# Optimization experiments

Hardware: AMD Instinct MI355X
Metric: run time of the kernel (lower is better)

## Reference

```python
import jax, jax.numpy as jnp
import numpy as np

# MoE config (mirrors init_kwargs)
E = 8        # num_experts
K = 2        # num_experts_per_tok
H = 1024     # hidden_size
F = 2816     # moe_intermediate_size
B, S = 2, 512
NORM_TOPK = True


def setup_inputs() -> dict:
    key = jax.random.key(0)
    ks = jax.random.split(key, 5)
    x = jax.random.normal(ks[0], (B, S, H), dtype=jnp.float32)
    router_w = jax.random.normal(ks[1], (E, H), dtype=jnp.float32) * 0.02   # nn.Linear(H, E).weight
    gate_proj = jax.random.normal(ks[2], (E, H, F), dtype=jnp.float32) * 0.02
    up_proj = jax.random.normal(ks[3], (E, H, F), dtype=jnp.float32) * 0.02
    down_proj = jax.random.normal(ks[4], (E, F, H), dtype=jnp.float32) * 0.02
    return {"x": x, "router_w": router_w, "gate_proj": gate_proj,
            "up_proj": up_proj, "down_proj": down_proj}


def reference(x, router_w, gate_proj, up_proj, down_proj):
    b, s, h = x.shape
    xf = x.reshape(-1, h)                                    # [T, H]
    # Router: softmax over experts, top-k selection mask
    logits = xf @ router_w.T                                 # [T, E]
    probs = jax.nn.softmax(logits, axis=-1)
    topk_p, topk_i = jax.lax.top_k(probs, K)                 # [T, K]
    routing_map = jax.nn.one_hot(topk_i, E, dtype=probs.dtype).sum(axis=1)  # [T, E] 0/1
    if NORM_TOPK:
        probs = probs / topk_p.sum(-1, keepdims=True)
    weight = probs * routing_map                             # [T, E]; zero for unselected experts
    # Per-expert SwiGLU FFN; combine weighted by routing prob.
    # Dense-masked formulation: mathematically identical to the original
    # gather -> per-expert GEMM -> scatter_add, since weight==0 for unrouted pairs.
    g = jnp.einsum('th,ehf->tef', xf, gate_proj)             # [T, E, F]
    u = jnp.einsum('th,ehf->tef', xf, up_proj)               # [T, E, F]
    m = jax.nn.silu(g) * u                                   # [T, E, F]
    out = jnp.einsum('tef,efh,te->th', m, down_proj, weight) # [T, H]
    return out.reshape(b, s, h)
```

## Files before the change

kernel.cpp:

```cpp
#include <hip/hip_runtime.h>

#define HD 1024
#define FD 2816
#define NE 8
#define NT 1024
#define NSLOT (NT * 2)
#define BMG 320

typedef short short8 __attribute__((ext_vector_type(8)));
typedef short short4v __attribute__((ext_vector_type(4)));
typedef float f32x4 __attribute__((ext_vector_type(4)));

typedef __attribute__((address_space(3))) unsigned lds_u32;
typedef __attribute__((address_space(1))) const unsigned glb_u32;

__device__ __forceinline__ void glds16(const void* g, void* l) {
  __builtin_amdgcn_global_load_lds((glb_u32*)g, (lds_u32*)l, 16, 0, 0);
}

__device__ __forceinline__ short f2bf(float f) {
  unsigned u = __builtin_bit_cast(unsigned, f);
  u += 0x7FFFu + ((u >> 16) & 1u);
  return (short)(u >> 16);
}
__device__ __forceinline__ int imin(int a, int b) { return a < b ? a : b; }

__global__ void router_kernel(const float* __restrict__ x,
                              const float* __restrict__ rw,
                              int* __restrict__ counts,
                              int* __restrict__ tok_i,
                              float* __restrict__ tok_w) {
  const int t = blockIdx.x;
  const int lane = threadIdx.x;
  const float* px = x + (size_t)t * HD;
  float acc[NE];
#pragma unroll
  for (int e = 0; e < NE; e++) acc[e] = 0.f;
  for (int h = lane; h < HD; h += 64) {
    float xv = px[h];
#pragma unroll
    for (int e = 0; e < NE; e++) acc[e] += xv * rw[e * HD + h];
  }
#pragma unroll
  for (int e = 0; e < NE; e++) {
#pragma unroll
    for (int off = 32; off > 0; off >>= 1)
      acc[e] += __shfl_xor(acc[e], off, 64);
  }
  if (lane == 0) {
    float mx = acc[0];
#pragma unroll
    for (int e = 1; e < NE; e++) mx = fmaxf(mx, acc[e]);
    float ex[NE];
#pragma unroll
    for (int e = 0; e < NE; e++) ex[e] = __expf(acc[e] - mx);
    int i1 = 0;
#pragma unroll
    for (int e = 1; e < NE; e++) if (ex[e] > ex[i1]) i1 = e;
    int i2 = (i1 == 0) ? 1 : 0;
#pragma unroll
    for (int e = 0; e < NE; e++) if (e != i1 && ex[e] > ex[i2]) i2 = e;
    float inv = 1.f / (ex[i1] + ex[i2]);
    tok_i[t * 2 + 0] = i1; tok_w[t * 2 + 0] = ex[i1] * inv;
    tok_i[t * 2 + 1] = i2; tok_w[t * 2 + 1] = ex[i2] * inv;
    atomicAdd(&counts[i1], 1);
    atomicAdd(&counts[i2], 1);
  }
}

__global__ void scan_kernel(const int* __restrict__ counts,
                            int* __restrict__ bases,
                            int* __restrict__ cursor) {
  if (threadIdx.x == 0) {
    int s = 0;
    for (int e = 0; e < NE; e++) { bases[e] = s; cursor[e] = s; s += counts[e]; }
    bases[NE] = s;
  }
}

__global__ void fill_kernel(const int* __restrict__ tok_i,
                            const float* __restrict__ tok_w,
                            int* __restrict__ cursor,
                            int* __restrict__ slot_token,
                            float* __restrict__ slot_w,
                            int* __restrict__ slot_of) {
  int t = blockIdx.x * 256 + threadIdx.x;
  if (t >= NT) return;
#pragma unroll
  for (int k = 0; k < 2; k++) {
    int e = tok_i[t * 2 + k];
    int pos = atomicAdd(&cursor[e], 1);
    slot_token[pos] = t;
    slot_w[pos] = tok_w[t * 2 + k];
    slot_of[t * 2 + k] = pos;
  }
}

__global__ void gather_kernel(const float* __restrict__ x,
                              const int* __restrict__ slot_token,
                              short* __restrict__ xg) {
  const int slot = blockIdx.x;
  const int tok = slot_token[slot];
  const int t = threadIdx.x;
  const int p = (slot >> 1) & 7;
  f32x4 v = *(const f32x4*)(x + (size_t)tok * HD + t * 4);
  short4v s;
#pragma unroll
  for (int j = 0; j < 4; j++) s[j] = f2bf(v[j]);
  *(short4v*)&xg[(size_t)slot * HD + (t >> 4) * 64 +
                 ((((t >> 1) & 7) ^ p) << 3) + ((t & 1) << 2)] = s;
}

__global__ __launch_bounds__(512, 2) void gateup_kernel(
    const short* __restrict__ xg, const float* __restrict__ gate_w,
    const float* __restrict__ up_w, const int* __restrict__ bases,
    short* __restrict__ m_out) {
  const int e = blockIdx.z;
  const int b0 = bases[e];
  const int ne = bases[e + 1] - b0;
  const int row0 = blockIdx.y * BMG;
  if (row0 >= ne) return;
  const int n0 = blockIdx.x * 64;
  const int CB = b0 + row0;

  __shared__ short As[2][BMG * 64];
  __shared__ short Bs[2][2][64 * 64];

  const int tid = threadIdx.x;
  const int lane = tid & 63, wid = tid >> 6;

  const short* asrc[5];
#pragma unroll
  for (int j = 0; j < 5; j++) {
    int i = j * 512 + tid;
    int row = i >> 3, c = i & 7;
    int slot = b0 + imin(row0 + row, ne - 1);
    asrc[j] = xg + (size_t)slot * HD + c * 8;
  }

  const int mat = tid >> 8;
  const int r = tid & 255;
  const int fq = r & 15, kq = r >> 4;
  const float* wsel = (mat ? up_w : gate_w) + (size_t)e * HD * FD + n0 + fq * 4;

  const int wm = wid >> 1, wn = wid & 1;
  const int l15 = lane & 15, l4 = lane >> 4;

  f32x4 accG[5][2], accU[5][2];
#pragma unroll
  for (int mi = 0; mi < 5; mi++)
#pragma unroll
    for (int ni = 0; ni < 2; ni++) { accG[mi][ni] = (f32x4)0.f; accU[mi][ni] = (f32x4)0.f; }

  f32x4 bv[4];

  auto stageA = [&](int buf, int k0) {
#pragma unroll
    for (int j = 0; j < 5; j++)
      glds16(asrc[j] + k0, &As[buf][(j * 512 + wid * 64) * 8]);
  };
  auto loadB = [&](int k0) {
#pragma unroll
    for (int kk = 0; kk < 4; kk++)
      bv[kk] = *(const f32x4*)(wsel + (size_t)(k0 + kq * 4 + kk) * FD);
  };
  auto writeB = [&](int buf) {
    short* Bd = &Bs[buf][mat][0];
#pragma unroll
    for (int ff = 0; ff < 4; ff++) {
      int n = fq * 4 + ff;
      short4v wv;
#pragma unroll
      for (int kk = 0; kk < 4; kk++) wv[kk] = f2bf(bv[kk][ff]);
      *(short4v*)&Bd[n * 64 + (((kq >> 1) ^ ((n >> 1) & 7)) << 3) +
                     ((kq & 1) << 2)] = wv;
    }
  };

  const int NTL = HD / 64;
  stageA(0, 0); loadB(0); writeB(0);
  stageA(1, 64); loadB(64);
  __syncthreads();

  for (int t = 0; t < NTL; t++) {
    const int cur = t & 1;
#pragma unroll
    for (int kk = 0; kk < 2; kk++) {
      short8 a[5], bg[2], bu[2];
#pragma unroll
      for (int mi = 0; mi < 5; mi++) {
        int R = wm * 80 + mi * 16 + l15;
        int sw = ((kk * 4 + l4) ^ (((CB + R) >> 1) & 7)) << 3;
        a[mi] = *(const short8*)&As[cur][R * 64 + sw];
      }
#pragma unroll
      for (int ni = 0; ni < 2; ni++) {
        int n = wn * 32 + ni * 16 + l15;
        int sw = ((kk * 4 + l4) ^ ((n >> 1) & 7)) << 3;
        bg[ni] = *(const short8*)&Bs[cur][0][n * 64 + sw];
        bu[ni] = *(const short8*)&Bs[cur][1][n * 64 + sw];
      }
#pragma unroll
      for (int mi = 0; mi < 5; mi++)
#pragma unroll
        for (int ni = 0; ni < 2; ni++) {
          accG[mi][ni] = __builtin_amdgcn_mfma_f32_16x16x32_bf16(a[mi], bg[ni], accG[mi][ni], 0, 0, 0);
          accU[mi][ni] = __builtin_amdgcn_mfma_f32_16x16x32_bf16(a[mi], bu[ni], accU[mi][ni], 0, 0, 0);
        }
    }
    if (t + 1 < NTL) writeB(cur ^ 1);
    __syncthreads();
    if (t + 2 < NTL) { stageA(cur, (t + 2) * 64); loadB((t + 2) * 64); }
  }

#pragma unroll
  for (int mi = 0; mi < 5; mi++)
#pragma unroll
    for (int ni = 0; ni < 2; ni++)
#pragma unroll
      for (int rr = 0; rr < 4; rr++) {
        int row = row0 + wm * 80 + mi * 16 + l4 * 4 + rr;
        if (row < ne) {
          int slot = b0 + row;
          float g = accG[mi][ni][rr];
          float u = accU[mi][ni][rr];
          float mv = (g / (1.f + __expf(-g))) * u;
          int psl = (slot >> 1) & 7;
          int cidx = (wn * 4 + ni * 2 + (l15 >> 3)) ^ psl;
          m_out[(size_t)slot * FD + n0 + (cidx << 3) + (l15 & 7)] = f2bf(mv);
        }
      }
}

__global__ __launch_bounds__(512, 2) void down_kernel(
    const short* __restrict__ m_in, const float* __restrict__ down_w,
    const int* __restrict__ bases, const float* __restrict__ slot_w,
    float* __restrict__ out_slot) {
  const int e = blockIdx.z;
  const int b0 = bases[e];
  const int ne = bases[e + 1] - b0;
  const int row0 = blockIdx.y * BMG;
  if (row0 >= ne) return;
  const int n0 = blockIdx.x * 64;
  const int CB = b0 + row0;

  __shared__ short As[2][BMG * 64];
  __shared__ short Bs[2][64 * 64];

  const int tid = threadIdx.x;
  const int lane = tid & 63, wid = tid >> 6;

  const short* asrc[5];
#pragma unroll
  for (int j = 0; j < 5; j++) {
    int i = j * 512 + tid;
    int row = i >> 3, c = i & 7;
    int slot = b0 + imin(row0 + row, ne - 1);
    asrc[j] = m_in + (size_t)slot * FD + c * 8;
  }

  const int fq = tid & 15, kq = (tid >> 4) & 15;
  const float* wb = down_w + (size_t)e * FD * HD + n0 + fq * 4;

  const int wm = wid >> 1, wn = wid & 1;
  const int l15 = lane & 15, l4 = lane >> 4;

  f32x4 acc[5][2];
#pragma unroll
  for (int mi = 0; mi < 5; mi++)
#pragma unroll
    for (int ni = 0; ni < 2; ni++) acc[mi][ni] = (f32x4)0.f;

  f32x4 bv[4];

  auto stageA = [&](int buf, int k0) {
#pragma unroll
    for (int j = 0; j < 5; j++)
      glds16(asrc[j] + k0, &As[buf][(j * 512 + wid * 64) * 8]);
  };
  auto loadB = [&](int k0) {
    if (tid < 256) {
#pragma unroll
      for (int kk = 0; kk < 4; kk++)
        bv[kk] = *(const f32x4*)(wb + (size_t)(k0 + kq * 4 + kk) * HD);
    }
  };
  auto writeB = [&](int buf) {
    if (tid < 256) {
#pragma unroll
      for (int ff = 0; ff < 4; ff++) {
        int n = fq * 4 + ff;
        short4v wv;
#pragma unroll
        for (int kk = 0; kk < 4; kk++) wv[kk] = f2bf(bv[kk][ff]);
        *(short4v*)&Bs[buf][n * 64 + (((kq >> 1) ^ ((n >> 1) & 7)) << 3) +
                            ((kq & 1) << 2)] = wv;
      }
    }
  };

  const int NTL = FD / 64;
  stageA(0, 0); loadB(0); writeB(0);
  stageA(1, 64); loadB(64);
  __syncthreads();

  for (int t = 0; t < NTL; t++) {
    const int cur = t & 1;
#pragma unroll
    for (int kk = 0; kk < 2; kk++) {
      short8 a[5], bf[2];
#pragma unroll
      for (int mi = 0; mi < 5; mi++) {
        int R = wm * 80 + mi * 16 + l15;
        int sw = ((kk * 4 + l4) ^ (((CB + R) >> 1) & 7)) << 3;
        a[mi] = *(const short8*)&As[cur][R * 64 + sw];
      }
#pragma unroll
      for (int ni = 0; ni < 2; ni++) {
        int n = wn * 32 + ni * 16 + l15;
        int sw = ((kk * 4 + l4) ^ ((n >> 1) & 7)) << 3;
        bf[ni] = *(const short8*)&Bs[cur][n * 64 + sw];
      }
#pragma unroll
      for (int mi = 0; mi < 5; mi++)
#pragma unroll
        for (int ni = 0; ni < 2; ni++)
          acc[mi][ni] = __builtin_amdgcn_mfma_f32_16x16x32_bf16(a[mi], bf[ni], acc[mi][ni], 0, 0, 0);
    }
    if (t + 1 < NTL) writeB(cur ^ 1);
    __syncthreads();
    if (t + 2 < NTL) { stageA(cur, (t + 2) * 64); loadB((t + 2) * 64); }
  }

#pragma unroll
  for (int mi = 0; mi < 5; mi++)
#pragma unroll
    for (int ni = 0; ni < 2; ni++)
#pragma unroll
      for (int rr = 0; rr < 4; rr++) {
        int row = row0 + wm * 80 + mi * 16 + l4 * 4 + rr;
        if (row < ne) {
          int slot = b0 + row;
          out_slot[(size_t)slot * HD + n0 + wn * 32 + ni * 16 + l15] =
              acc[mi][ni][rr] * slot_w[slot];
        }
      }
}

__global__ void combine_kernel(const float* __restrict__ out_slot,
                               const int* __restrict__ slot_of,
                               float* __restrict__ out) {
  const int t = blockIdx.x;
  const int s0 = slot_of[t * 2];
  const int s1 = slot_of[t * 2 + 1];
  const int i = threadIdx.x * 4;
  f32x4 a = *(const f32x4*)(out_slot + (size_t)s0 * HD + i);
  f32x4 b = *(const f32x4*)(out_slot + (size_t)s1 * HD + i);
  f32x4 c = a + b;
  *(f32x4*)(out + (size_t)t * HD + i) = c;
}

extern "C" void kernel_launch(void* const* d_in, const int* in_sizes, int n_in,
                              void* d_out, int out_size, void* d_ws,
                              size_t ws_size, hipStream_t stream) {
  const float* x = (const float*)d_in[0];
  const float* rw = (const float*)d_in[1];
  const float* gw = (const float*)d_in[2];
  const float* uw = (const float*)d_in[3];
  const float* dw = (const float*)d_in[4];
  float* out = (float*)d_out;

  char* ws = (char*)d_ws;
  int* counts = (int*)(ws + 0);
  int* cursor = (int*)(ws + 64);
  int* bases = (int*)(ws + 128);
  int* tok_i = (int*)(ws + 256);
  float* tok_w = (float*)(ws + 8448);
  int* slot_token = (int*)(ws + 16640);
  float* slot_w = (float*)(ws + 24832);
  int* slot_of = (int*)(ws + 33024);
  short* xg = (short*)(ws + 41216);
  short* m_buf = (short*)(ws + 4235520);
  float* out_slot = (float*)(ws + 15769856);

  hipMemsetAsync(counts, 0, 64, stream);
  router_kernel<<<NT, 64, 0, stream>>>(x, rw, counts, tok_i, tok_w);
  scan_kernel<<<1, 64, 0, stream>>>(counts, bases, cursor);
  fill_kernel<<<NT / 256, 256, 0, stream>>>(tok_i, tok_w, cursor, slot_token,
                                            slot_w, slot_of);
  gather_kernel<<<NSLOT, 256, 0, stream>>>(x, slot_token, xg);
  gateup_kernel<<<dim3(FD / 64, 4, NE), 512, 0, stream>>>(xg, gw, uw, bases,
                                                          m_buf);
  down_kernel<<<dim3(HD / 64, 4, NE), 512, 0, stream>>>(m_buf, dw, bases,
                                                        slot_w, out_slot);
  combine_kernel<<<NT, 256, 0, stream>>>(out_slot, slot_of, out);
}
```

Measured before the change: 211.7 us.

## Shrink GEMM tiles to 128/64 rows with K=32 steps and new LDS swizzle

Replaces the 320-row, K=64, 512-thread tiles in both expert GEMMs with smaller 256-thread blocks: 128 rows for gate/up and 64 rows for down, with K advancing 32 per iteration. The grid grows to 16 and 32 row-blocks per expert, which gives many more CTAs for uneven expert sizes and wastes fewer padded rows. The gather and intermediate layouts become plain row-major, and a new pair-of-rows XOR swizzle is applied in LDS instead. In exchange, fp32 weights are re-read and converted once per row-block, which greatly increases weight traffic, and the shorter K steps mean more barriers per unit of work.

```diff
diff --git a/kernel.cpp b/kernel.cpp
--- a/kernel.cpp
+++ b/kernel.cpp
@@ -5,11 +5,11 @@
 #define NE 8
 #define NT 1024
 #define NSLOT (NT * 2)
-#define BMG 320
 
 typedef short short8 __attribute__((ext_vector_type(8)));
 typedef short short4v __attribute__((ext_vector_type(4)));
 typedef float f32x4 __attribute__((ext_vector_type(4)));
+typedef float f32x2 __attribute__((ext_vector_type(2)));
 
 typedef __attribute__((address_space(3))) unsigned lds_u32;
 typedef __attribute__((address_space(1))) const unsigned glb_u32;
@@ -102,243 +102,229 @@
   const int slot = blockIdx.x;
   const int tok = slot_token[slot];
   const int t = threadIdx.x;
-  const int p = (slot >> 1) & 7;
   f32x4 v = *(const f32x4*)(x + (size_t)tok * HD + t * 4);
   short4v s;
 #pragma unroll
   for (int j = 0; j < 4; j++) s[j] = f2bf(v[j]);
-  *(short4v*)&xg[(size_t)slot * HD + (t >> 4) * 64 +
-                 ((((t >> 1) & 7) ^ p) << 3) + ((t & 1) << 2)] = s;
-}
-
-__global__ __launch_bounds__(512, 2) void gateup_kernel(
+  *(short4v*)&xg[(size_t)slot * HD + t * 4] = s;
+}
+
+
+__global__ __launch_bounds__(256, 2) void gateup_kernel(
     const short* __restrict__ xg, const float* __restrict__ gate_w,
     const float* __restrict__ up_w, const int* __restrict__ bases,
     short* __restrict__ m_out) {
   const int e = blockIdx.z;
   const int b0 = bases[e];
   const int ne = bases[e + 1] - b0;
-  const int row0 = blockIdx.y * BMG;
+  const int row0 = blockIdx.y * 128;
   if (row0 >= ne) return;
   const int n0 = blockIdx.x * 64;
-  const int CB = b0 + row0;
-
-  __shared__ short As[2][BMG * 64];
-  __shared__ short Bs[2][2][64 * 64];
+
+  __shared__ short As[2][128 * 32];
+  __shared__ short Bs[2][2][64 * 32];
 
   const int tid = threadIdx.x;
   const int lane = tid & 63, wid = tid >> 6;
-
-  const short* asrc[5];
-#pragma unroll
-  for (int j = 0; j < 5; j++) {
-    int i = j * 512 + tid;
-    int row = i >> 3, c = i & 7;
-    int slot = b0 + imin(row0 + row, ne - 1);
+  const int l15 = lane & 15, l4 = lane >> 4;
+  const int wm = wid >> 1, wn = wid & 1;
+
+  const short* asrc[2];
+#pragma unroll
+  for (int j = 0; j < 2; j++) {
+    int i = j * 256 + tid;
+    int p = i >> 3;
+    int v = (i & 7) ^ (p & 7);
+    int rl = 2 * p + (v >> 2), c = v & 3;
+    int slot = b0 + imin(row0 + rl, ne - 1);
     asrc[j] = xg + (size_t)slot * HD + c * 8;
   }
 
-  const int mat = tid >> 8;
-  const int r = tid & 255;
-  const int fq = r & 15, kq = r >> 4;
-  const float* wsel = (mat ? up_w : gate_w) + (size_t)e * HD * FD + n0 + fq * 4;
-
-  const int wm = wid >> 1, wn = wid & 1;
-  const int l15 = lane & 15, l4 = lane >> 4;
-
-  f32x4 accG[5][2], accU[5][2];
-#pragma unroll
-  for (int mi = 0; mi < 5; mi++)
+  const int mat = tid >> 7;
+  const int rb = tid & 127;
+  const int fp = rb & 31, kq = rb >> 5;
+  const float* wsel = (mat ? up_w : gate_w) + (size_t)e * HD * FD + n0 + fp * 2;
+
+  f32x4 accG[4][2], accU[4][2];
+#pragma unroll
+  for (int mi = 0; mi < 4; mi++)
 #pragma unroll
     for (int ni = 0; ni < 2; ni++) { accG[mi][ni] = (f32x4)0.f; accU[mi][ni] = (f32x4)0.f; }
 
-  f32x4 bv[4];
+  f32x2 bv[8];
 
   auto stageA = [&](int buf, int k0) {
 #pragma unroll
-    for (int j = 0; j < 5; j++)
-      glds16(asrc[j] + k0, &As[buf][(j * 512 + wid * 64) * 8]);
+    for (int j = 0; j < 2; j++)
+      glds16(asrc[j] + k0, &As[buf][j * 2048 + wid * 512]);
   };
   auto loadB = [&](int k0) {
 #pragma unroll
-    for (int kk = 0; kk < 4; kk++)
-      bv[kk] = *(const f32x4*)(wsel + (size_t)(k0 + kq * 4 + kk) * FD);
+    for (int i = 0; i < 8; i++)
+      bv[i] = *(const f32x2*)(wsel + (size_t)(k0 + kq * 8 + i) * FD);
   };
   auto writeB = [&](int buf) {
     short* Bd = &Bs[buf][mat][0];
 #pragma unroll
-    for (int ff = 0; ff < 4; ff++) {
-      int n = fq * 4 + ff;
-      short4v wv;
-#pragma unroll
-      for (int kk = 0; kk < 4; kk++) wv[kk] = f2bf(bv[kk][ff]);
-      *(short4v*)&Bd[n * 64 + (((kq >> 1) ^ ((n >> 1) & 7)) << 3) +
-                     ((kq & 1) << 2)] = wv;
-    }
-  };
-
-  const int NTL = HD / 64;
+    for (int ff = 0; ff < 2; ff++) {
+      int jslot = ((ff << 2) | kq) ^ (fp & 7);
+      short8 s;
+#pragma unroll
+      for (int i = 0; i < 8; i++) s[i] = f2bf(bv[i][ff]);
+      *(short8*)&Bd[fp * 64 + jslot * 8] = s;
+    }
+  };
+
+  const int NTL = HD / 32;
   stageA(0, 0); loadB(0); writeB(0);
-  stageA(1, 64); loadB(64);
+  stageA(1, 32); loadB(32);
   __syncthreads();
 
   for (int t = 0; t < NTL; t++) {
     const int cur = t & 1;
-#pragma unroll
-    for (int kk = 0; kk < 2; kk++) {
-      short8 a[5], bg[2], bu[2];
-#pragma unroll
-      for (int mi = 0; mi < 5; mi++) {
-        int R = wm * 80 + mi * 16 + l15;
-        int sw = ((kk * 4 + l4) ^ (((CB + R) >> 1) & 7)) << 3;
-        a[mi] = *(const short8*)&As[cur][R * 64 + sw];
+    short8 a[4], bg[2], bu[2];
+#pragma unroll
+    for (int mi = 0; mi < 4; mi++) {
+      int R = wm * 64 + mi * 16 + l15;
+      a[mi] = *(const short8*)&As[cur][(R >> 1) * 64 +
+                ((((R & 1) << 2) | l4) ^ ((R >> 1) & 7)) * 8];
+    }
+#pragma unroll
+    for (int ni = 0; ni < 2; ni++) {
+      int n = wn * 32 + ni * 16 + l15;
+      int off = (n >> 1) * 64 + ((((n & 1) << 2) | l4) ^ ((n >> 1) & 7)) * 8;
+      bg[ni] = *(const short8*)&Bs[cur][0][off];
+      bu[ni] = *(const short8*)&Bs[cur][1][off];
+    }
+#pragma unroll
+    for (int mi = 0; mi < 4; mi++)
+#pragma unroll
+      for (int ni = 0; ni < 2; ni++) {
+        accG[mi][ni] = __builtin_amdgcn_mfma_f32_16x16x32_bf16(a[mi], bg[ni], accG[mi][ni], 0, 0, 0);
+        accU[mi][ni] = __builtin_amdgcn_mfma_f32_16x16x32_bf16(a[mi], bu[ni], accU[mi][ni], 0, 0, 0);
       }
-#pragma unroll
-      for (int ni = 0; ni < 2; ni++) {
-        int n = wn * 32 + ni * 16 + l15;
-        int sw = ((kk * 4 + l4) ^ ((n >> 1) & 7)) << 3;
-        bg[ni] = *(const short8*)&Bs[cur][0][n * 64 + sw];
-        bu[ni] = *(const short8*)&Bs[cur][1][n * 64 + sw];
-      }
-#pragma unroll
-      for (int mi = 0; mi < 5; mi++)
-#pragma unroll
-        for (int ni = 0; ni < 2; ni++) {
-          accG[mi][ni] = __builtin_amdgcn_mfma_f32_16x16x32_bf16(a[mi], bg[ni], accG[mi][ni], 0, 0, 0);
-          accU[mi][ni] = __builtin_amdgcn_mfma_f32_16x16x32_bf16(a[mi], bu[ni], accU[mi][ni], 0, 0, 0);
-        }
-    }
     if (t + 1 < NTL) writeB(cur ^ 1);
     __syncthreads();
-    if (t + 2 < NTL) { stageA(cur, (t + 2) * 64); loadB((t + 2) * 64); }
-  }
-
-#pragma unroll
-  for (int mi = 0; mi < 5; mi++)
+    if (t + 2 < NTL) { stageA(cur, (t + 2) * 32); loadB((t + 2) * 32); }
+  }
+
+#pragma unroll
+  for (int mi = 0; mi < 4; mi++)
 #pragma unroll
     for (int ni = 0; ni < 2; ni++)
 #pragma unroll
       for (int rr = 0; rr < 4; rr++) {
-        int row = row0 + wm * 80 + mi * 16 + l4 * 4 + rr;
+        int row = row0 + wm * 64 + mi * 16 + l4 * 4 + rr;
         if (row < ne) {
           int slot = b0 + row;
           float g = accG[mi][ni][rr];
           float u = accU[mi][ni][rr];
           float mv = (g / (1.f + __expf(-g))) * u;
-          int psl = (slot >> 1) & 7;
-          int cidx = (wn * 4 + ni * 2 + (l15 >> 3)) ^ psl;
-          m_out[(size_t)slot * FD + n0 + (cidx << 3) + (l15 & 7)] = f2bf(mv);
+          m_out[(size_t)slot * FD + n0 + wn * 32 + ni * 16 + l15] = f2bf(mv);
         }
       }
 }
 
-__global__ __launch_bounds__(512, 2) void down_kernel(
+__global__ __launch_bounds__(256, 2) void down_kernel(
     const short* __restrict__ m_in, const float* __restrict__ down_w,
     const int* __restrict__ bases, const float* __restrict__ slot_w,
     float* __restrict__ out_slot) {
   const int e = blockIdx.z;
   const int b0 = bases[e];
   const int ne = bases[e + 1] - b0;
-  const int row0 = blockIdx.y * BMG;
+  const int row0 = blockIdx.y * 64;
   if (row0 >= ne) return;
   const int n0 = blockIdx.x * 64;
-  const int CB = b0 + row0;
-
-  __shared__ short As[2][BMG * 64];
-  __shared__ short Bs[2][64 * 64];
+
+  __shared__ short As[2][64 * 32];
+  __shared__ short Bs[2][64 * 32];
 
   const int tid = threadIdx.x;
   const int lane = tid & 63, wid = tid >> 6;
-
-  const short* asrc[5];
-#pragma unroll
-  for (int j = 0; j < 5; j++) {
-    int i = j * 512 + tid;
-    int row = i >> 3, c = i & 7;
-    int slot = b0 + imin(row0 + row, ne - 1);
-    asrc[j] = m_in + (size_t)slot * FD + c * 8;
-  }
-
-  const int fq = tid & 15, kq = (tid >> 4) & 15;
-  const float* wb = down_w + (size_t)e * FD * HD + n0 + fq * 4;
-
+  const int l15 = lane & 15, l4 = lane >> 4;
   const int wm = wid >> 1, wn = wid & 1;
-  const int l15 = lane & 15, l4 = lane >> 4;
-
-  f32x4 acc[5][2];
-#pragma unroll
-  for (int mi = 0; mi < 5; mi++)
+
+  const short* asrc;
+  {
+    int p = tid >> 3;
+    int v = (tid & 7) ^ (p & 7);
+    int rl = 2 * p + (v >> 2), c = v & 3;
+    int slot = b0 + imin(row0 + rl, ne - 1);
+    asrc = m_in + (size_t)slot * FD + c * 8;
+  }
+
+  const int rb = tid & 127;
+  const int fp = rb & 31, kq = rb >> 5;
+  const float* wb = down_w + (size_t)e * FD * HD + n0 + fp * 2;
+
+  f32x4 acc[2][2];
+#pragma unroll
+  for (int mi = 0; mi < 2; mi++)
 #pragma unroll
     for (int ni = 0; ni < 2; ni++) acc[mi][ni] = (f32x4)0.f;
 
-  f32x4 bv[4];
+  f32x2 bv[8];
 
   auto stageA = [&](int buf, int k0) {
-#pragma unroll
-    for (int j = 0; j < 5; j++)
-      glds16(asrc[j] + k0, &As[buf][(j * 512 + wid * 64) * 8]);
+    glds16(asrc + k0, &As[buf][wid * 512]);
   };
   auto loadB = [&](int k0) {
-    if (tid < 256) {
-#pragma unroll
-      for (int kk = 0; kk < 4; kk++)
-        bv[kk] = *(const f32x4*)(wb + (size_t)(k0 + kq * 4 + kk) * HD);
+    if (tid < 128) {
+#pragma unroll
+      for (int i = 0; i < 8; i++)
+        bv[i] = *(const f32x2*)(wb + (size_t)(k0 + kq * 8 + i) * HD);
     }
   };
   auto writeB = [&](int buf) {
-    if (tid < 256) {
-#pragma unroll
-      for (int ff = 0; ff < 4; ff++) {
-        int n = fq * 4 + ff;
-        short4v wv;
-#pragma unroll
-        for (int kk = 0; kk < 4; kk++) wv[kk] = f2bf(bv[kk][ff]);
-        *(short4v*)&Bs[buf][n * 64 + (((kq >> 1) ^ ((n >> 1) & 7)) << 3) +
-                            ((kq & 1) << 2)] = wv;
+    if (tid < 128) {
+#pragma unroll
+      for (int ff = 0; ff < 2; ff++) {
+        int jslot = ((ff << 2) | kq) ^ (fp & 7);
+        short8 s;
+#pragma unroll
+        for (int i = 0; i < 8; i++) s[i] = f2bf(bv[i][ff]);
+        *(short8*)&Bs[buf][fp * 64 + jslot * 8] = s;
       }
     }
   };
 
-  const int NTL = FD / 64;
+  const int NTL = FD / 32;
   stageA(0, 0); loadB(0); writeB(0);
-  stageA(1, 64); loadB(64);
+  stageA(1, 32); loadB(32);
   __syncthreads();
 
   for (int t = 0; t < NTL; t++) {
     const int cur = t & 1;
-#pragma unroll
-    for (int kk = 0; kk < 2; kk++) {
-      short8 a[5], bf[2];
-#pragma unroll
-      for (int mi = 0; mi < 5; mi++) {
-        int R = wm * 80 + mi * 16 + l15;
-        int sw = ((kk * 4 + l4) ^ (((CB + R) >> 1) & 7)) << 3;
-        a[mi] = *(const short8*)&As[cur][R * 64 + sw];
-      }
-#pragma unroll
-      for (int ni = 0; ni < 2; ni++) {
-        int n = wn * 32 + ni * 16 + l15;
-        int sw = ((kk * 4 + l4) ^ ((n >> 1) & 7)) << 3;
-        bf[ni] = *(const short8*)&Bs[cur][n * 64 + sw];
-      }
-#pragma unroll
-      for (int mi = 0; mi < 5; mi++)
-#pragma unroll
-        for (int ni = 0; ni < 2; ni++)
-          acc[mi][ni] = __builtin_amdgcn_mfma_f32_16x16x32_bf16(a[mi], bf[ni], acc[mi][ni], 0, 0, 0);
-    }
+    short8 a[2], bf[2];
+#pragma unroll
+    for (int mi = 0; mi < 2; mi++) {
+      int R = wm * 32 + mi * 16 + l15;
+      a[mi] = *(const short8*)&As[cur][(R >> 1) * 64 +
+                ((((R & 1) << 2) | l4) ^ ((R >> 1) & 7)) * 8];
+    }
+#pragma unroll
+    for (int ni = 0; ni < 2; ni++) {
+      int n = wn * 32 + ni * 16 + l15;
+      bf[ni] = *(const short8*)&Bs[cur][(n >> 1) * 64 +
+                ((((n & 1) << 2) | l4) ^ ((n >> 1) & 7)) * 8];
+    }
+#pragma unroll
+    for (int mi = 0; mi < 2; mi++)
+#pragma unroll
+      for (int ni = 0; ni < 2; ni++)
+        acc[mi][ni] = __builtin_amdgcn_mfma_f32_16x16x32_bf16(a[mi], bf[ni], acc[mi][ni], 0, 0, 0);
     if (t + 1 < NTL) writeB(cur ^ 1);
     __syncthreads();
-    if (t + 2 < NTL) { stageA(cur, (t + 2) * 64); loadB((t + 2) * 64); }
-  }
-
-#pragma unroll
-  for (int mi = 0; mi < 5; mi++)
+    if (t + 2 < NTL) { stageA(cur, (t + 2) * 32); loadB((t + 2) * 32); }
+  }
+
+#pragma unroll
+  for (int mi = 0; mi < 2; mi++)
 #pragma unroll
     for (int ni = 0; ni < 2; ni++)
 #pragma unroll
       for (int rr = 0; rr < 4; rr++) {
-        int row = row0 + wm * 80 + mi * 16 + l4 * 4 + rr;
+        int row = row0 + wm * 32 + mi * 16 + l4 * 4 + rr;
         if (row < ne) {
           int slot = b0 + row;
           out_slot[(size_t)slot * HD + n0 + wn * 32 + ni * 16 + l15] =
@@ -389,9 +375,9 @@
   fill_kernel<<<NT / 256, 256, 0, stream>>>(tok_i, tok_w, cursor, slot_token,
                                             slot_w, slot_of);
   gather_kernel<<<NSLOT, 256, 0, stream>>>(x, slot_token, xg);
-  gateup_kernel<<<dim3(FD / 64, 4, NE), 512, 0, stream>>>(xg, gw, uw, bases,
-                                                          m_buf);
-  down_kernel<<<dim3(HD / 64, 4, NE), 512, 0, stream>>>(m_buf, dw, bases,
-                                                        slot_w, out_slot);
+  gateup_kernel<<<dim3(FD / 64, 16, NE), 256, 0, stream>>>(xg, gw, uw, bases,
+                                                           m_buf);
+  down_kernel<<<dim3(HD / 64, 32, NE), 256, 0, stream>>>(m_buf, dw, bases,
+                                                         slot_w, out_slot);
   combine_kernel<<<NT, 256, 0, stream>>>(out_slot, slot_of, out);
 }
```

After: 276.7 us. 30.7% more time.
